# Kernel optimization log

Measured on AMD Instinct MI355X. Metric: run time of the kernel, lower is better.

## Reference

```python
import jax, jax.numpy as jnp
import numpy as np

EMBED = 1024
HEADS = 16
HDIM = 64
FFN = 4 * EMBED
EPS = 1e-5


def setup_inputs() -> dict:
    key = jax.random.key(0)
    ks = jax.random.split(key, 12)
    def lin(k, fan_in, shape):
        b = 1.0 / np.sqrt(fan_in)
        return jax.random.uniform(k, shape, jnp.float32, -b, b)
    return {
        "x": jax.random.normal(ks[0], (4, 2048, EMBED), jnp.float32),
        "Wq": lin(ks[1], EMBED, (EMBED, HEADS * HDIM)),
        "Wk": lin(ks[2], EMBED, (EMBED, HEADS * HDIM)),
        "Wv": lin(ks[3], EMBED, (EMBED, HEADS * HDIM)),
        "Wo": lin(ks[4], HEADS * HDIM, (HEADS * HDIM, EMBED)),
        "ln1_g": jnp.ones((EMBED,), jnp.float32),
        "ln1_b": jnp.zeros((EMBED,), jnp.float32),
        "ln2_g": jnp.ones((EMBED,), jnp.float32),
        "ln2_b": jnp.zeros((EMBED,), jnp.float32),
        "W1": lin(ks[5], EMBED, (EMBED, FFN)),
        "b1": lin(ks[6], EMBED, (FFN,)),
        "W2": lin(ks[7], FFN, (FFN, EMBED)),
        "b2": lin(ks[8], FFN, (EMBED,)),
    }


def _layer_norm(x, g, b):
    mu = jnp.mean(x, axis=-1, keepdims=True)
    var = jnp.var(x, axis=-1, keepdims=True)
    return (x - mu) * jax.lax.rsqrt(var + EPS) * g + b


def reference(x, Wq, Wk, Wv, Wo, ln1_g, ln1_b, ln2_g, ln2_b, W1, b1, W2, b2):
    B, S, _ = x.shape
    residual = x
    h = _layer_norm(x, ln1_g, ln1_b)
    # project and split heads: [B, H, S, Dh]
    q = (h @ Wq).reshape(B, S, HEADS, HDIM).transpose(0, 2, 1, 3)
    k = (h @ Wk).reshape(B, S, HEADS, HDIM).transpose(0, 2, 1, 3)
    v = (h @ Wv).reshape(B, S, HEADS, HDIM).transpose(0, 2, 1, 3)
    scale = HDIM ** -0.5
    scores = jnp.einsum("bhqd,bhkd->bhqk", q, k) * scale
    # causal mask (upper triangle excluded above diagonal -> -inf)
    mask = jnp.triu(jnp.ones((S, S), bool), k=1)
    scores = jnp.where(mask, -jnp.inf, scores)
    attn = jax.nn.softmax(scores, axis=-1)
    out = jnp.einsum("bhqk,bhkd->bhqd", attn, v)
    out = out.transpose(0, 2, 1, 3).reshape(B, S, HEADS * HDIM)
    x = residual + out @ Wo
    residual = x
    h = _layer_norm(x, ln2_g, ln2_b)
    h = jax.nn.gelu(h @ W1 + b1, approximate=False) @ W2 + b2
    return residual + h
```

## Files before the change

### kernel.cpp

```cpp
#include <hip/hip_runtime.h>
#include <hip/hip_bf16.h>
#include <math.h>

typedef __bf16 bf16;
typedef bf16 bf16x8 __attribute__((ext_vector_type(8)));
typedef bf16 bf16x4 __attribute__((ext_vector_type(4)));
typedef float f32x4 __attribute__((ext_vector_type(4)));

#define ROWS 8192
#define EMB  1024
#define NH   16
#define HD   64
#define FFN  4096
#define QKVN 3072
#define SEQ  2048

__device__ __forceinline__ void gl2lds16(const bf16* g, bf16* l) {
  __builtin_amdgcn_global_load_lds((const __attribute__((address_space(1))) void*)g,
                                   (__attribute__((address_space(3))) void*)l, 16, 0, 0);
}

__global__ void transpose_cast(const float* __restrict__ W, bf16* __restrict__ Wt,
                               int K, int N, float scale) {
  __shared__ float tile[32][33];
  const int n0 = blockIdx.x * 32, k0 = blockIdx.y * 32;
  const int tx = threadIdx.x & 31, ty = threadIdx.x >> 5;
#pragma unroll
  for (int i = 0; i < 32; i += 8)
    tile[ty + i][tx] = W[(size_t)(k0 + ty + i) * N + n0 + tx];
  __syncthreads();
#pragma unroll
  for (int i = 0; i < 32; i += 8)
    Wt[(size_t)(n0 + ty + i) * K + k0 + tx] = (bf16)(tile[tx][ty + i] * scale);
}

__global__ void transpose_cast4(const float* __restrict__ W0, const float* __restrict__ W1,
                                const float* __restrict__ W2, const float* __restrict__ W3,
                                bf16* __restrict__ dst) {
  __shared__ float tile[32][33];
  const int z = blockIdx.z;
  const float* W = (z == 0) ? W0 : (z == 1) ? W1 : (z == 2) ? W2 : W3;
  const float scale = (z == 0) ? 0.125f : 1.0f;
  bf16* Wt = dst + (size_t)z * EMB * EMB;
  const int n0 = blockIdx.x * 32, k0 = blockIdx.y * 32;
  const int tx = threadIdx.x & 31, ty = threadIdx.x >> 5;
#pragma unroll
  for (int i = 0; i < 32; i += 8)
    tile[ty + i][tx] = W[(size_t)(k0 + ty + i) * EMB + n0 + tx];
  __syncthreads();
#pragma unroll
  for (int i = 0; i < 32; i += 8)
    Wt[(size_t)(n0 + ty + i) * EMB + k0 + tx] = (bf16)(tile[tx][ty + i] * scale);
}

__global__ void v_transpose(const bf16* __restrict__ qkv, bf16* __restrict__ vt) {
  __shared__ bf16 tile[32][33];
  const int s0 = blockIdx.x * 32, d0 = blockIdx.y * 32, bh = blockIdx.z;
  const int b = bh >> 4, h = bh & 15;
  const int tx = threadIdx.x & 31, ty = threadIdx.x >> 5;
#pragma unroll
  for (int i = 0; i < 32; i += 8)
    tile[ty + i][tx] = qkv[(size_t)(b * SEQ + s0 + ty + i) * QKVN + 2 * EMB + h * HD + d0 + tx];
  __syncthreads();
#pragma unroll
  for (int i = 0; i < 32; i += 8)
    vt[(size_t)(bh * HD + d0 + ty + i) * SEQ + s0 + tx] = tile[tx][ty + i];
}

__global__ void layernorm_bf16(const float* __restrict__ x, const float* __restrict__ g,
                               const float* __restrict__ b, bf16* __restrict__ out) {
  const int row = blockIdx.x;
  const int t = threadIdx.x;
  const float4 v = ((const float4*)(x + (size_t)row * EMB))[t];
  float s = v.x + v.y + v.z + v.w;
  float ss = v.x * v.x + v.y * v.y + v.z * v.z + v.w * v.w;
#pragma unroll
  for (int off = 32; off; off >>= 1) {
    s += __shfl_down(s, off);
    ss += __shfl_down(ss, off);
  }
  __shared__ float sbuf[8];
  const int wave = t >> 6, lane = t & 63;
  if (lane == 0) { sbuf[wave] = s; sbuf[4 + wave] = ss; }
  __syncthreads();
  if (t == 0) {
    float S = sbuf[0] + sbuf[1] + sbuf[2] + sbuf[3];
    float SS = sbuf[4] + sbuf[5] + sbuf[6] + sbuf[7];
    float mu = S * (1.0f / EMB);
    float var = SS * (1.0f / EMB) - mu * mu;
    sbuf[0] = mu;
    sbuf[1] = rsqrtf(var + 1e-5f);
  }
  __syncthreads();
  const float mu = sbuf[0], rs = sbuf[1];
  const float4 gv = ((const float4*)g)[t];
  const float4 bv = ((const float4*)b)[t];
  bf16x4 o;
  o[0] = (bf16)((v.x - mu) * rs * gv.x + bv.x);
  o[1] = (bf16)((v.y - mu) * rs * gv.y + bv.y);
  o[2] = (bf16)((v.z - mu) * rs * gv.z + bv.z);
  o[3] = (bf16)((v.w - mu) * rs * gv.w + bv.w);
  *(bf16x4*)(out + (size_t)row * EMB + t * 4) = o;
}

template <int EPI, int N_, int K_>
__global__ __launch_bounds__(256, 2) void gemm_bt(
    const bf16* __restrict__ A, const bf16* __restrict__ Bt, void* __restrict__ C,
    const float* __restrict__ bias, const float* __restrict__ resid) {
  constexpr int N = N_, K = K_;
  __shared__ __align__(16) bf16 As[128 * 64];
  __shared__ __align__(16) bf16 Bs[128 * 64];
  const int tid = threadIdx.x;
  const int lane = tid & 63;
  const int wave = tid >> 6;
  const int wm = (wave >> 1) * 64;
  const int wn = (wave & 1) * 64;
  constexpr int tn = N / 128;
  const int lin = blockIdx.y * tn + blockIdx.x;
  const int xcd = lin & 7;
  const int idx = lin >> 3;
  const int m0 = (xcd * 8 + (idx & 7)) * 128;
  const int n0 = (idx >> 3) * 128;
  const int quad = lane >> 4;
  const int l16 = lane & 15;
  const int srow8 = lane >> 3;
  const int scol = ((lane & 7) ^ srow8) * 8;
  const int xr = l16 & 7;

  const bf16* ap = A + (size_t)(m0 + wave * 32 + srow8) * K + scol;
  const bf16* bp = Bt + (size_t)(n0 + wave * 32 + srow8) * K + scol;
  bf16* const as0 = &As[wave * 32 * 64];
  bf16* const bs0 = &Bs[wave * 32 * 64];

  f32x4 acc[4][4] = {};

  for (int kt = 0; kt < K; kt += 64) {
    __syncthreads();
#pragma unroll
    for (int q = 0; q < 4; q++) {
      gl2lds16(ap + q * 8 * K, as0 + q * 8 * 64);
      gl2lds16(bp + q * 8 * K, bs0 + q * 8 * 64);
    }
    ap += 64;
    bp += 64;
    __syncthreads();
#pragma unroll
    for (int h = 0; h < 2; h++) {
      const int cp = ((h * 4 + quad) ^ xr) * 8;
      bf16x8 af[4], bfr[4];
#pragma unroll
      for (int i = 0; i < 4; i++)
        af[i] = *(const bf16x8*)&As[(wm + i * 16 + l16) * 64 + cp];
#pragma unroll
      for (int j = 0; j < 4; j++)
        bfr[j] = *(const bf16x8*)&Bs[(wn + j * 16 + l16) * 64 + cp];
#pragma unroll
      for (int i = 0; i < 4; i++)
#pragma unroll
        for (int j = 0; j < 4; j++)
          acc[i][j] = __builtin_amdgcn_mfma_f32_16x16x32_bf16(af[i], bfr[j], acc[i][j], 0, 0, 0);
    }
  }

#pragma unroll
  for (int i = 0; i < 4; i++)
#pragma unroll
    for (int j = 0; j < 4; j++)
#pragma unroll
      for (int r = 0; r < 4; r++) {
        const int row = m0 + wm + i * 16 + quad * 4 + r;
        const int col = n0 + wn + j * 16 + l16;
        const size_t idx2 = (size_t)row * N + col;
        float v = acc[i][j][r];
        if (EPI == 0) {
          ((bf16*)C)[idx2] = (bf16)v;
        } else if (EPI == 1) {
          ((float*)C)[idx2] = v + resid[idx2];
        } else if (EPI == 2) {
          v += bias[col];
          const float u = 1.5957691216f * (v + 0.044715f * v * v * v);
          v = v / (1.0f + __expf(-u));
          ((bf16*)C)[idx2] = (bf16)v;
        } else {
          ((float*)C)[idx2] = v + bias[col] + resid[idx2];
        }
      }
}

__global__ __launch_bounds__(256, 6) void flash_attn(
    const bf16* __restrict__ qkv, const bf16* __restrict__ vt, bf16* __restrict__ out) {
  const int bid = blockIdx.x;
  const int xcd = bid & 7;
  const int idx = bid >> 3;
  const int pr = idx & 15;
  const int bh = xcd + ((idx >> 4) << 3);
  const int b = bh >> 4, h = bh & 15;
  const int tid = threadIdx.x;
  const int lane = tid & 63, wave = tid >> 6;
  const int quad = lane >> 4, l16 = lane & 15;

  __shared__ __align__(16) bf16 Ks[64 * 64];
  __shared__ __align__(16) bf16 Vts[64 * 64];
  __shared__ __align__(16) bf16 Ps[4][16][72];

  const size_t rowbase = (size_t)b * SEQ;
  const int s8 = (lane >> 3) & 7;
  const int cs = ((lane & 7) ^ s8) * 8;
  const int xk = l16 & 7;
  const bf16* kbase = qkv + rowbase * QKVN + EMB + h * HD;
  const bf16* vbase = vt + (size_t)(bh * HD) * SEQ;

#pragma unroll 1
  for (int half = 0; half < 2; half++) {
    const int qt = half ? pr : 31 - pr;
    const int qrow_a = qt * 64 + wave * 16 + l16;
    const bf16* qptr = qkv + (rowbase + qrow_a) * QKVN + h * HD;
    const bf16x8 qf0 = *(const bf16x8*)(qptr + quad * 8);
    const bf16x8 qf1 = *(const bf16x8*)(qptr + 32 + quad * 8);
    f32x4 o0 = {}, o1 = {}, o2 = {}, o3 = {};
    f32x4 lsum = {};
    const int qrow_c = qt * 64 + wave * 16 + quad * 4;

    const bf16* kp = kbase + (size_t)(wave * 8 + s8) * QKVN + cs;
    const bf16* vp = vbase + (size_t)(wave * 8 + s8) * SEQ + cs;

#pragma unroll 1
    for (int kt = 0; kt <= qt; kt++) {
      __syncthreads();
      gl2lds16(kp + (size_t)kt * 64 * QKVN, &Ks[(wave * 8) * 64]);
      gl2lds16(kp + (size_t)(kt * 64 + 32) * QKVN, &Ks[(32 + wave * 8) * 64]);
      gl2lds16(vp + kt * 64, &Vts[(wave * 8) * 64]);
      gl2lds16(vp + (size_t)32 * SEQ + kt * 64, &Vts[(32 + wave * 8) * 64]);
      __syncthreads();

      if (kt < qt) {
#pragma unroll
        for (int j = 0; j < 4; j++) {
          const int rr = (j * 16 + l16) * 64;
          const bf16x8 kf0 = *(const bf16x8*)&Ks[rr + (quad ^ xk) * 8];
          const bf16x8 kf1 = *(const bf16x8*)&Ks[rr + ((4 + quad) ^ xk) * 8];
          f32x4 a = {};
          a = __builtin_amdgcn_mfma_f32_16x16x32_bf16(qf0, kf0, a, 0, 0, 0);
          a = __builtin_amdgcn_mfma_f32_16x16x32_bf16(qf1, kf1, a, 0, 0, 0);
#pragma unroll
          for (int r = 0; r < 4; r++) {
            const float pj = __expf(a[r]);
            lsum[r] += pj;
            Ps[wave][quad * 4 + r][j * 16 + l16] = (bf16)pj;
          }
        }
      } else {
#pragma unroll
        for (int j = 0; j < 4; j++) {
          if (j > wave) {
#pragma unroll
            for (int r = 0; r < 4; r++)
              Ps[wave][quad * 4 + r][j * 16 + l16] = (bf16)0.0f;
          } else {
            const int rr = (j * 16 + l16) * 64;
            const bf16x8 kf0 = *(const bf16x8*)&Ks[rr + (quad ^ xk) * 8];
            const bf16x8 kf1 = *(const bf16x8*)&Ks[rr + ((4 + quad) ^ xk) * 8];
            f32x4 a = {};
            a = __builtin_amdgcn_mfma_f32_16x16x32_bf16(qf0, kf0, a, 0, 0, 0);
            a = __builtin_amdgcn_mfma_f32_16x16x32_bf16(qf1, kf1, a, 0, 0, 0);
            if (j == wave) {
#pragma unroll
              for (int r = 0; r < 4; r++) {
                const float v = (l16 > quad * 4 + r) ? -INFINITY : a[r];
                const float pj = __expf(v);
                lsum[r] += pj;
                Ps[wave][quad * 4 + r][j * 16 + l16] = (bf16)pj;
              }
            } else {
#pragma unroll
              for (int r = 0; r < 4; r++) {
                const float pj = __expf(a[r]);
                lsum[r] += pj;
                Ps[wave][quad * 4 + r][j * 16 + l16] = (bf16)pj;
              }
            }
          }
        }
      }

      const bf16x8 af0 = *(const bf16x8*)&Ps[wave][l16][quad * 8];
      const bf16x8 af1 = *(const bf16x8*)&Ps[wave][l16][32 + quad * 8];
#pragma unroll
      for (int j = 0; j < 4; j++) {
        const int rr = (j * 16 + l16) * 64;
        const bf16x8 vf0 = *(const bf16x8*)&Vts[rr + (quad ^ xk) * 8];
        const bf16x8 vf1 = *(const bf16x8*)&Vts[rr + ((4 + quad) ^ xk) * 8];
        f32x4& oj = (j == 0) ? o0 : (j == 1) ? o1 : (j == 2) ? o2 : o3;
        oj = __builtin_amdgcn_mfma_f32_16x16x32_bf16(af0, vf0, oj, 0, 0, 0);
        oj = __builtin_amdgcn_mfma_f32_16x16x32_bf16(af1, vf1, oj, 0, 0, 0);
      }
    }

#pragma unroll
    for (int r = 0; r < 4; r++) {
      float ls = lsum[r];
      ls += __shfl_xor(ls, 1);
      ls += __shfl_xor(ls, 2);
      ls += __shfl_xor(ls, 4);
      ls += __shfl_xor(ls, 8);
      const float iv = 1.0f / ls;
      bf16* op = out + (rowbase + qrow_c + r) * EMB + h * HD;
      op[0 + l16] = (bf16)(o0[r] * iv);
      op[16 + l16] = (bf16)(o1[r] * iv);
      op[32 + l16] = (bf16)(o2[r] * iv);
      op[48 + l16] = (bf16)(o3[r] * iv);
    }
  }
}

extern "C" void kernel_launch(void* const* d_in, const int* in_sizes, int n_in,
                              void* d_out, int out_size, void* d_ws, size_t ws_size,
                              hipStream_t stream) {
  const float* x     = (const float*)d_in[0];
  const float* Wq    = (const float*)d_in[1];
  const float* Wk    = (const float*)d_in[2];
  const float* Wv    = (const float*)d_in[3];
  const float* Wo    = (const float*)d_in[4];
  const float* ln1_g = (const float*)d_in[5];
  const float* ln1_b = (const float*)d_in[6];
  const float* ln2_g = (const float*)d_in[7];
  const float* ln2_b = (const float*)d_in[8];
  const float* W1    = (const float*)d_in[9];
  const float* b1    = (const float*)d_in[10];
  const float* W2    = (const float*)d_in[11];
  const float* b2    = (const float*)d_in[12];
  float* out = (float*)d_out;

  bf16* p = (bf16*)d_ws;
  bf16* wqkv_t = p;                 p += (size_t)QKVN * EMB;
  bf16* wo_t   = p;                 p += (size_t)EMB * EMB;
  bf16* w1_t   = p;                 p += (size_t)FFN * EMB;
  bf16* w2_t   = p;                 p += (size_t)EMB * FFN;
  bf16* h      = p;                 p += (size_t)ROWS * EMB;
  bf16* qkv    = p;                 p += (size_t)ROWS * QKVN;
  bf16* attn_o = p;                 p += (size_t)ROWS * EMB;
  bf16* ffn1   = p;
  bf16* vt     = h;

  transpose_cast4<<<dim3(32, 32, 4), 256, 0, stream>>>(Wq, Wk, Wv, Wo, wqkv_t);
  transpose_cast<<<dim3(128, 32), 256, 0, stream>>>(W1, w1_t, EMB, FFN, 1.0f);
  transpose_cast<<<dim3(32, 128), 256, 0, stream>>>(W2, w2_t, FFN, EMB, 1.0f);

  layernorm_bf16<<<ROWS, 256, 0, stream>>>(x, ln1_g, ln1_b, h);

  gemm_bt<0, QKVN, EMB><<<dim3(QKVN / 128, ROWS / 128), 256, 0, stream>>>(
      h, wqkv_t, qkv, nullptr, nullptr);

  v_transpose<<<dim3(SEQ / 32, HD / 32, 64), 256, 0, stream>>>(qkv, vt);

  flash_attn<<<1024, 256, 0, stream>>>(qkv, vt, attn_o);

  gemm_bt<1, EMB, EMB><<<dim3(EMB / 128, ROWS / 128), 256, 0, stream>>>(
      attn_o, wo_t, out, nullptr, x);

  layernorm_bf16<<<ROWS, 256, 0, stream>>>(out, ln2_g, ln2_b, h);

  gemm_bt<2, FFN, EMB><<<dim3(FFN / 128, ROWS / 128), 256, 0, stream>>>(
      h, w1_t, ffn1, b1, nullptr);

  gemm_bt<3, EMB, FFN><<<dim3(EMB / 128, ROWS / 128), 256, 0, stream>>>(
      ffn1, w2_t, out, b2, out);
}
```

Measured before the change: 454.9 us.

## Fuse V transpose into QKV GEMM epilogue and use wave-per-row layernorm

The QKV GEMM gains an epilogue that writes the V section directly in transposed per-head layout, which removes the separate v_transpose kernel and its extra read and write of V. The transposed V buffer now reuses the W1 transpose scratch, so the W1/W2 weight casts move after attention. Layernorm is rewritten so that one wavefront handles a whole row with xor-shuffle reductions, dropping shared memory and block barriers. The transposed V stores are narrow and strided, which may cost some store efficiency.

```diff
diff --git a/kernel.cpp b/kernel.cpp
--- a/kernel.cpp
+++ b/kernel.cpp
@@ -53,60 +53,46 @@
     Wt[(size_t)(n0 + ty + i) * EMB + k0 + tx] = (bf16)(tile[tx][ty + i] * scale);
 }
 
-__global__ void v_transpose(const bf16* __restrict__ qkv, bf16* __restrict__ vt) {
-  __shared__ bf16 tile[32][33];
-  const int s0 = blockIdx.x * 32, d0 = blockIdx.y * 32, bh = blockIdx.z;
-  const int b = bh >> 4, h = bh & 15;
-  const int tx = threadIdx.x & 31, ty = threadIdx.x >> 5;
-#pragma unroll
-  for (int i = 0; i < 32; i += 8)
-    tile[ty + i][tx] = qkv[(size_t)(b * SEQ + s0 + ty + i) * QKVN + 2 * EMB + h * HD + d0 + tx];
-  __syncthreads();
-#pragma unroll
-  for (int i = 0; i < 32; i += 8)
-    vt[(size_t)(bh * HD + d0 + ty + i) * SEQ + s0 + tx] = tile[tx][ty + i];
-}
-
-__global__ void layernorm_bf16(const float* __restrict__ x, const float* __restrict__ g,
-                               const float* __restrict__ b, bf16* __restrict__ out) {
-  const int row = blockIdx.x;
-  const int t = threadIdx.x;
-  const float4 v = ((const float4*)(x + (size_t)row * EMB))[t];
-  float s = v.x + v.y + v.z + v.w;
-  float ss = v.x * v.x + v.y * v.y + v.z * v.z + v.w * v.w;
+__global__ __launch_bounds__(256) void layernorm_bf16(
+    const float* __restrict__ x, const float* __restrict__ g,
+    const float* __restrict__ b, bf16* __restrict__ out) {
+  const int row = blockIdx.x * 4 + (threadIdx.x >> 6);
+  const int lane = threadIdx.x & 63;
+  const float4* xr = (const float4*)(x + (size_t)row * EMB);
+  float4 v[4];
+  float s = 0.f, ss = 0.f;
+#pragma unroll
+  for (int k = 0; k < 4; k++) {
+    v[k] = xr[lane + 64 * k];
+    s += v[k].x + v[k].y + v[k].z + v[k].w;
+    ss += v[k].x * v[k].x + v[k].y * v[k].y + v[k].z * v[k].z + v[k].w * v[k].w;
+  }
 #pragma unroll
   for (int off = 32; off; off >>= 1) {
-    s += __shfl_down(s, off);
-    ss += __shfl_down(ss, off);
-  }
-  __shared__ float sbuf[8];
-  const int wave = t >> 6, lane = t & 63;
-  if (lane == 0) { sbuf[wave] = s; sbuf[4 + wave] = ss; }
-  __syncthreads();
-  if (t == 0) {
-    float S = sbuf[0] + sbuf[1] + sbuf[2] + sbuf[3];
-    float SS = sbuf[4] + sbuf[5] + sbuf[6] + sbuf[7];
-    float mu = S * (1.0f / EMB);
-    float var = SS * (1.0f / EMB) - mu * mu;
-    sbuf[0] = mu;
-    sbuf[1] = rsqrtf(var + 1e-5f);
-  }
-  __syncthreads();
-  const float mu = sbuf[0], rs = sbuf[1];
-  const float4 gv = ((const float4*)g)[t];
-  const float4 bv = ((const float4*)b)[t];
-  bf16x4 o;
-  o[0] = (bf16)((v.x - mu) * rs * gv.x + bv.x);
-  o[1] = (bf16)((v.y - mu) * rs * gv.y + bv.y);
-  o[2] = (bf16)((v.z - mu) * rs * gv.z + bv.z);
-  o[3] = (bf16)((v.w - mu) * rs * gv.w + bv.w);
-  *(bf16x4*)(out + (size_t)row * EMB + t * 4) = o;
+    s += __shfl_xor(s, off);
+    ss += __shfl_xor(ss, off);
+  }
+  const float mu = s * (1.0f / EMB);
+  const float rs = rsqrtf(ss * (1.0f / EMB) - mu * mu + 1e-5f);
+  bf16* orow = out + (size_t)row * EMB;
+#pragma unroll
+  for (int k = 0; k < 4; k++) {
+    const float4 gv = ((const float4*)g)[lane + 64 * k];
+    const float4 bv = ((const float4*)b)[lane + 64 * k];
+    bf16x4 o;
+    o[0] = (bf16)((v[k].x - mu) * rs * gv.x + bv.x);
+    o[1] = (bf16)((v[k].y - mu) * rs * gv.y + bv.y);
+    o[2] = (bf16)((v[k].z - mu) * rs * gv.z + bv.z);
+    o[3] = (bf16)((v[k].w - mu) * rs * gv.w + bv.w);
+    *(bf16x4*)(orow + (size_t)(lane + 64 * k) * 4) = o;
+  }
 }
 
 template <int EPI, int N_, int K_>
 __global__ __launch_bounds__(256, 2) void gemm_bt(
     const bf16* __restrict__ A, const bf16* __restrict__ Bt, void* __restrict__ C,
-    const float* __restrict__ bias, const float* __restrict__ resid) {
+    const float* __restrict__ bias, const float* __restrict__ resid,
+    bf16* __restrict__ vt) {
   constexpr int N = N_, K = K_;
   __shared__ __align__(16) bf16 As[128 * 64];
   __shared__ __align__(16) bf16 Bs[128 * 64];
@@ -162,6 +148,26 @@
     }
   }
 
+  if (EPI == 4 && n0 >= 2 * EMB) {
+#pragma unroll
+    for (int i = 0; i < 4; i++)
+#pragma unroll
+      for (int j = 0; j < 4; j++) {
+        const int col = n0 + wn + j * 16 + l16;
+        const int c2 = col - 2 * EMB;
+        const int h_ = c2 >> 6, d = c2 & 63;
+        const int row0 = m0 + wm + i * 16 + quad * 4;
+        const int b_ = row0 >> 11, s = row0 & (SEQ - 1);
+        bf16x4 o;
+        o[0] = (bf16)acc[i][j][0];
+        o[1] = (bf16)acc[i][j][1];
+        o[2] = (bf16)acc[i][j][2];
+        o[3] = (bf16)acc[i][j][3];
+        *(bf16x4*)(vt + ((size_t)((b_ * 16 + h_) * 64 + d)) * SEQ + s) = o;
+      }
+    return;
+  }
+
 #pragma unroll
   for (int i = 0; i < 4; i++)
 #pragma unroll
@@ -172,7 +178,7 @@
         const int col = n0 + wn + j * 16 + l16;
         const size_t idx2 = (size_t)row * N + col;
         float v = acc[i][j][r];
-        if (EPI == 0) {
+        if (EPI == 0 || EPI == 4) {
           ((bf16*)C)[idx2] = (bf16)v;
         } else if (EPI == 1) {
           ((float*)C)[idx2] = v + resid[idx2];
@@ -340,29 +346,28 @@
   bf16* qkv    = p;                 p += (size_t)ROWS * QKVN;
   bf16* attn_o = p;                 p += (size_t)ROWS * EMB;
   bf16* ffn1   = p;
-  bf16* vt     = h;
+  bf16* vt     = w1_t;
 
   transpose_cast4<<<dim3(32, 32, 4), 256, 0, stream>>>(Wq, Wk, Wv, Wo, wqkv_t);
+
+  layernorm_bf16<<<ROWS / 4, 256, 0, stream>>>(x, ln1_g, ln1_b, h);
+
+  gemm_bt<4, QKVN, EMB><<<dim3(QKVN / 128, ROWS / 128), 256, 0, stream>>>(
+      h, wqkv_t, qkv, nullptr, nullptr, vt);
+
+  flash_attn<<<1024, 256, 0, stream>>>(qkv, vt, attn_o);
+
   transpose_cast<<<dim3(128, 32), 256, 0, stream>>>(W1, w1_t, EMB, FFN, 1.0f);
   transpose_cast<<<dim3(32, 128), 256, 0, stream>>>(W2, w2_t, FFN, EMB, 1.0f);
 
-  layernorm_bf16<<<ROWS, 256, 0, stream>>>(x, ln1_g, ln1_b, h);
-
-  gemm_bt<0, QKVN, EMB><<<dim3(QKVN / 128, ROWS / 128), 256, 0, stream>>>(
-      h, wqkv_t, qkv, nullptr, nullptr);
-
-  v_transpose<<<dim3(SEQ / 32, HD / 32, 64), 256, 0, stream>>>(qkv, vt);
-
-  flash_attn<<<1024, 256, 0, stream>>>(qkv, vt, attn_o);
-
   gemm_bt<1, EMB, EMB><<<dim3(EMB / 128, ROWS / 128), 256, 0, stream>>>(
-      attn_o, wo_t, out, nullptr, x);
-
-  layernorm_bf16<<<ROWS, 256, 0, stream>>>(out, ln2_g, ln2_b, h);
+      attn_o, wo_t, out, nullptr, x, nullptr);
+
+  layernorm_bf16<<<ROWS / 4, 256, 0, stream>>>(out, ln2_g, ln2_b, h);
 
   gemm_bt<2, FFN, EMB><<<dim3(FFN / 128, ROWS / 128), 256, 0, stream>>>(
-      h, w1_t, ffn1, b1, nullptr);
+      h, w1_t, ffn1, b1, nullptr, nullptr);
 
   gemm_bt<3, EMB, FFN><<<dim3(EMB / 128, ROWS / 128), 256, 0, stream>>>(
-      ffn1, w2_t, out, b2, out);
-}
+      ffn1, w2_t, out, b2, out, nullptr);
+}
```

After: 465.2 us. 1.02x slower.
